# Kernel optimization log

Hardware: AMD Instinct MI355X
Metric: run time of the kernel (lower is better)

## Reference

```python
import jax, jax.numpy as jnp
import numpy as np

B, N, D, H, FF, K, L = 8, 4096, 128, 8, 512, 16, 2
DH = D // H
EPS = 1e-5


def setup_inputs() -> dict:
    key = jax.random.key(0)
    ks = jax.random.split(key, 32)
    s = 0.02
    inp = {
        "x": jax.random.normal(ks[0], (B, N, 8), dtype=jnp.float32),
        "xyz_w": jax.random.normal(ks[1], (D, 3), jnp.float32) * s,
        "xyz_b": jnp.zeros((D,), jnp.float32),
        "ohe_w": jax.random.normal(ks[2], (D, 5), jnp.float32) * s,
        "ohe_b": jnp.zeros((D,), jnp.float32),
        # per-layer transformer params stacked on leading L axis
        "in_proj_w": jax.random.normal(ks[3], (L, 3 * D, D), jnp.float32) * s,
        "in_proj_b": jnp.zeros((L, 3 * D), jnp.float32),
        "out_proj_w": jax.random.normal(ks[4], (L, D, D), jnp.float32) * s,
        "out_proj_b": jnp.zeros((L, D), jnp.float32),
        "ln1_w": jnp.ones((L, D), jnp.float32),
        "ln1_b": jnp.zeros((L, D), jnp.float32),
        "lin1_w": jax.random.normal(ks[5], (L, FF, D), jnp.float32) * s,
        "lin1_b": jnp.zeros((L, FF), jnp.float32),
        "lin2_w": jax.random.normal(ks[6], (L, D, FF), jnp.float32) * s,
        "lin2_b": jnp.zeros((L, D), jnp.float32),
        "ln2_w": jnp.ones((L, D), jnp.float32),
        "ln2_b": jnp.zeros((L, D), jnp.float32),
        "fc1_w": jax.random.normal(ks[7], (FF, D), jnp.float32) * s,
        "fc1_b": jnp.zeros((FF,), jnp.float32),
        "fc2_w": jax.random.normal(ks[8], (1, FF), jnp.float32) * s,
        "fc2_b": jnp.zeros((1,), jnp.float32),
    }
    return inp


def _layer_norm(x, w, b):
    m = jnp.mean(x, -1, keepdims=True)
    v = jnp.mean((x - m) ** 2, -1, keepdims=True)
    return (x - m) * jax.lax.rsqrt(v + EPS) * w + b


def _knn_attention(xyz, feat):
    # squared euclidean distances preserve top-k ordering of cdist(p=2)
    d2 = jnp.sum((xyz[:, :, None, :] - xyz[:, None, :, :]) ** 2, -1)  # [B,N,N]
    _, idx = jax.lax.top_k(-d2, K + 1)  # ascending distance
    idx = idx[..., 1:]  # drop self -> [B,N,K]
    knn = jax.vmap(lambda f, i: f[i])(feat, idx)  # [B,N,K,D]
    scale = 1.0 / np.sqrt(D)
    scores = jnp.einsum('bnd,bnkd->bnk', feat, knn) * scale
    w = jax.nn.softmax(scores, -1)
    return jnp.einsum('bnk,bnkd->bnd', w, knn)


def _mha(x, in_w, in_b, out_w, out_b):
    qkv = x @ in_w.T + in_b  # [B,N,3D]
    q, k, v = jnp.split(qkv, 3, axis=-1)
    def heads(t):
        return t.reshape(B, N, H, DH).transpose(0, 2, 1, 3)  # [B,H,N,DH]
    q, k, v = heads(q), heads(k), heads(v)
    scores = jnp.einsum('bhqd,bhkd->bhqk', q, k) / np.sqrt(DH)
    a = jax.nn.softmax(scores, -1)
    o = jnp.einsum('bhqk,bhkd->bhqd', a, v).transpose(0, 2, 1, 3).reshape(B, N, D)
    return o @ out_w.T + out_b


def reference(x, xyz_w, xyz_b, ohe_w, ohe_b, in_proj_w, in_proj_b, out_proj_w,
              out_proj_b, ln1_w, ln1_b, lin1_w, lin1_b, lin2_w, lin2_b,
              ln2_w, ln2_b, fc1_w, fc1_b, fc2_w, fc2_b):
    xyz = x[:, :, :3]
    ohe = x[:, :, 3:8]
    feat = (xyz @ xyz_w.T + xyz_b) + (ohe @ ohe_w.T + ohe_b)  # [B,N,D]
    h = _knn_attention(xyz, feat)
    # post-norm TransformerEncoder (PyTorch default, relu, no dropout at eval)
    for l in range(L):
        a = _mha(h, in_proj_w[l], in_proj_b[l], out_proj_w[l], out_proj_b[l])
        h = _layer_norm(h + a, ln1_w[l], ln1_b[l])
        f = jax.nn.relu(h @ lin1_w[l].T + lin1_b[l]) @ lin2_w[l].T + lin2_b[l]
        h = _layer_norm(h + f, ln2_w[l], ln2_b[l])
    pooled = jnp.mean(h, axis=1)  # [B,D]
    out = jax.nn.sigmoid(jax.nn.relu(pooled @ fc1_w.T + fc1_b) @ fc2_w.T + fc2_b)
    return out
```

## Files before the change

### kernel.cpp

```cpp
#include <hip/hip_runtime.h>

#define Bq 8
#define Nq 4096
#define Dq 128
#define Hq 8
#define FFq 512
#define KNNq 16
#define Lq 2
#define DHq 16
#define EPSq 1e-5f

typedef _Float16 half4 __attribute__((ext_vector_type(4)));
typedef _Float16 half2t __attribute__((ext_vector_type(2)));
typedef float v4f __attribute__((ext_vector_type(4)));

static __device__ __forceinline__ half2t pkrtz(float a, float b) {
    return __builtin_bit_cast(half2t, __builtin_amdgcn_cvt_pkrtz(a, b));
}

__global__ __launch_bounds__(256) void prep_kernel(const float* __restrict__ x,
                                                   const float* __restrict__ xyz_w,
                                                   const float* __restrict__ xyz_b,
                                                   const float* __restrict__ ohe_w,
                                                   const float* __restrict__ ohe_b,
                                                   _Float16* __restrict__ feat16,
                                                   const float* __restrict__ ipw,
                                                   const float* __restrict__ opw,
                                                   const float* __restrict__ l1w,
                                                   const float* __restrict__ l2w,
                                                   _Float16* __restrict__ wb) {
    int bid = blockIdx.x;
    if (bid < 16384) {
        int i = bid * 256 + threadIdx.x;
        int d = i & 127;
        int t = i >> 7;
        const float* xr = x + (size_t)t * 8;
        float s = xyz_b[d] + ohe_b[d];
        s += xr[0] * xyz_w[d * 3 + 0] + xr[1] * xyz_w[d * 3 + 1] + xr[2] * xyz_w[d * 3 + 2];
        s += xr[3] * ohe_w[d * 5 + 0] + xr[4] * ohe_w[d * 5 + 1] + xr[5] * ohe_w[d * 5 + 2]
           + xr[6] * ohe_w[d * 5 + 3] + xr[7] * ohe_w[d * 5 + 4];
        feat16[i] = (_Float16)s;
    } else {
        int i = (bid - 16384) * 256 + threadIdx.x;
        float v;
        if (i < 98304) v = ipw[i];
        else if (i < 131072) v = opw[i - 98304];
        else if (i < 262144) v = l1w[i - 131072];
        else v = l2w[i - 262144];
        wb[i] = (_Float16)v;
    }
}

__global__ __launch_bounds__(512) void knn_kernel(const float* __restrict__ x, int* __restrict__ idx) {
    __shared__ __attribute__((aligned(16))) float sx[Nq];
    __shared__ __attribute__((aligned(16))) float sy[Nq];
    __shared__ __attribute__((aligned(16))) float sz[Nq];
    unsigned int (*md)[17] = (unsigned int (*)[17])sx;
    int b = blockIdx.y;
    int tid = threadIdx.x;
    for (int p = tid; p < Nq; p += 512) {
        const float* xr = x + ((size_t)b * Nq + p) * 8;
        sx[p] = xr[0]; sy[p] = xr[1]; sz[p] = xr[2];
    }
    __syncthreads();
    int qi = tid >> 3;
    int part = tid & 7;
    int n = blockIdx.x * 64 + qi;
    float qx = sx[n], qy = sy[n], qz = sz[n];
    unsigned int top[16];
#pragma unroll
    for (int i = 0; i < 16; i++) top[i] = 0xFFFFFFFFu;
    int j0 = part * 512;
    int rot = part;
    for (int bb = 0; bb < 32; bb++) {
        unsigned int c[16];
#pragma unroll
        for (int u = 0; u < 16; u++) {
            int j = j0 + ((bb * 16 + rot + u) & 511);
            float px = sx[j], py = sy[j], pz = sz[j];
            float dx = qx - px, dy = qy - py, dz = qz - pz;
            float d2 = fmaf(dx, dx, fmaf(dy, dy, dz * dz));
            unsigned int ky = (__float_as_uint(d2) & 0xFFFFF000u) | (unsigned int)j;
            c[u] = (j == n) ? 0xFFFFFFFFu : ky;
        }
#pragma unroll
        for (int kk = 2; kk <= 16; kk <<= 1) {
#pragma unroll
            for (int jj = 16 >> 1; jj > 0; jj >>= 1) {
                if (jj < kk) {
#pragma unroll
                    for (int i = 0; i < 16; i++) {
                        int l = i ^ jj;
                        if (l > i) {
                            unsigned int a0 = c[i], b0 = c[l];
                            unsigned int mn = a0 < b0 ? a0 : b0;
                            unsigned int mx = a0 < b0 ? b0 : a0;
                            bool up = ((i & kk) == 0);
                            c[i] = up ? mn : mx;
                            c[l] = up ? mx : mn;
                        }
                    }
                }
            }
        }
#pragma unroll
        for (int i = 0; i < 16; i++) {
            unsigned int a0 = top[i], b0 = c[15 - i];
            top[i] = a0 < b0 ? a0 : b0;
        }
#pragma unroll
        for (int d = 8; d >= 1; d >>= 1) {
#pragma unroll
            for (int i = 0; i < 16; i++) {
                if ((i & d) == 0) {
                    int l = i | d;
                    unsigned int a0 = top[i], b0 = top[l];
                    top[i] = a0 < b0 ? a0 : b0;
                    top[l] = a0 < b0 ? b0 : a0;
                }
            }
        }
    }
    __syncthreads();
#pragma unroll
    for (int i = 0; i < 16; i++) md[tid][i] = top[i];
    __syncthreads();
    if (part == 0) {
        unsigned int pall = 0;
        int* op = idx + ((size_t)b * Nq + n) * KNNq;
        int base_row = qi * 8;
#pragma unroll
        for (int s = 0; s < KNNq; s++) {
            unsigned int best = 0xFFFFFFFFu; int bp = 0;
#pragma unroll
            for (int p2 = 0; p2 < 8; p2++) {
                unsigned int ptr = (pall >> (p2 * 4)) & 15u;
                unsigned int v = md[base_row + p2][ptr];
                if (v < best) { best = v; bp = p2; }
            }
            op[s] = (int)(best & 4095u);
            pall += (1u << (bp * 4));
        }
    }
}

__global__ __launch_bounds__(256, 4) void knn_attn_kernel(const _Float16* __restrict__ feat16,
                                                          const int* __restrict__ idx,
                                                          _Float16* __restrict__ h16) {
    int wave = threadIdx.x >> 6;
    int lane = threadIdx.x & 63;
    int token = blockIdx.x * 4 + wave;
    int b = token >> 12;
    half2t fh = ((const half2t*)(feat16 + (size_t)token * Dq))[lane];
    float2 f = make_float2((float)fh[0], (float)fh[1]);
    const int* ip = idx + (size_t)token * KNNq;
    int jj[KNNq];
#pragma unroll
    for (int k = 0; k < KNNq; k++) jj[k] = ip[k];
    float2 g[KNNq];
#pragma unroll
    for (int k = 0; k < KNNq; k++) {
        half2t gh = ((const half2t*)(feat16 + (((size_t)b << 12) + jj[k]) * Dq))[lane];
        g[k] = make_float2((float)gh[0], (float)gh[1]);
    }
    float sc[KNNq];
#pragma unroll
    for (int k = 0; k < KNNq; k++) {
        float p = f.x * g[k].x + f.y * g[k].y;
#pragma unroll
        for (int m = 1; m < 64; m <<= 1) p += __shfl_xor(p, m);
        sc[k] = p * 0.088388347648318447f;
    }
    float mx = sc[0];
#pragma unroll
    for (int k = 1; k < KNNq; k++) mx = fmaxf(mx, sc[k]);
    float sum = 0.f;
#pragma unroll
    for (int k = 0; k < KNNq; k++) { sc[k] = __expf(sc[k] - mx); sum += sc[k]; }
    float inv = 1.f / sum;
    float o0 = 0.f, o1 = 0.f;
#pragma unroll
    for (int k = 0; k < KNNq; k++) { o0 += sc[k] * g[k].x; o1 += sc[k] * g[k].y; }
    ((half2t*)(h16 + (size_t)token * Dq))[lane] = pkrtz(o0 * inv, o1 * inv);
}

template <int MODE>
__global__ __launch_bounds__(256) void hgemm_kernel(const _Float16* __restrict__ A,
                                                    const _Float16* __restrict__ W,
                                                    const float* __restrict__ bias,
                                                    void* __restrict__ Cout,
                                                    int M, int Nc, int K) {
    int tid = threadIdx.x;
    int lane = tid & 63, w = tid >> 6;
    int l15 = lane & 15, l4 = lane >> 4;
    int m0 = blockIdx.y * 64 + w * 16;
    int n0 = blockIdx.x * 64;
    const _Float16* Ap = A + (size_t)(m0 + l15) * K + l4 * 4;
    const _Float16* Wp = W + (size_t)(n0 + l15) * K + l4 * 4;
    v4f acc[4] = {{0.f, 0.f, 0.f, 0.f}, {0.f, 0.f, 0.f, 0.f}, {0.f, 0.f, 0.f, 0.f}, {0.f, 0.f, 0.f, 0.f}};
    for (int ks = 0; ks < K; ks += 16) {
        half4 af = *(const half4*)(Ap + ks);
#pragma unroll
        for (int nt = 0; nt < 4; nt++) {
            half4 wf = *(const half4*)(Wp + (size_t)nt * 16 * K + ks);
            acc[nt] = __builtin_amdgcn_mfma_f32_16x16x16f16(wf, af, acc[nt], 0, 0, 0);
        }
    }
    int m = m0 + l15;
#pragma unroll
    for (int nt = 0; nt < 4; nt++) {
        int nb = n0 + nt * 16 + l4 * 4;
        float4 bv = *(const float4*)(bias + nb);
        float v0 = acc[nt][0] + bv.x, v1 = acc[nt][1] + bv.y;
        float v2 = acc[nt][2] + bv.z, v3 = acc[nt][3] + bv.w;
        int n_base = n0 + nt * 16;
        int sel = n_base >> 7;
        if (MODE == 2 && sel == 0) {
            v0 *= 0.36067376f; v1 *= 0.36067376f; v2 *= 0.36067376f; v3 *= 0.36067376f;
        }
        half2t lo = pkrtz(v0, v1);
        half2t hi = pkrtz(v2, v3);
        half4 hv; hv[0] = lo[0]; hv[1] = lo[1]; hv[2] = hi[0]; hv[3] = hi[1];
        if (sel < 2) {
            int hh = (n_base >> 4) & 7;
            size_t base = (size_t)sel * (64ull * Nq * 16)
                        + ((size_t)((m >> 12) * 8 + hh)) * (Nq * 16)
                        + (size_t)(m & 4095) * 16 + l4 * 4;
            *(half4*)((_Float16*)Cout + base) = hv;
        } else {
            int hh = (n_base >> 4) & 7;
            size_t vb = 2ull * 64 * Nq * 16
                      + ((size_t)((m >> 12) * 8 + hh)) * (16 * Nq)
                      + (size_t)(m & 4095);
            _Float16* vp = (_Float16*)Cout + vb + (size_t)(l4 * 4) * Nq;
            vp[0 * Nq] = hv[0]; vp[1 * Nq] = hv[1]; vp[2 * Nq] = hv[2]; vp[3 * Nq] = hv[3];
        }
    }
}

__global__ __launch_bounds__(256) void flash12_kernel(const _Float16* __restrict__ pk,
                                                      _Float16* __restrict__ out16) {
    __shared__ _Float16 Ks[2][64 * 20];
    __shared__ _Float16 Vs[2][16 * 66];
    int tid = threadIdx.x;
    int lane = tid & 63, w = tid >> 6;
    int bh = blockIdx.y;
    const _Float16* Qb = pk + (size_t)bh * (Nq * 16);
    const _Float16* Kb = pk + (size_t)(64 + bh) * (Nq * 16);
    const _Float16* Vt = pk + 2ull * 64 * Nq * 16 + (size_t)bh * (16 * Nq);
    int q0 = blockIdx.x * 128 + w * 32;
    int l15 = lane & 15, l4 = lane >> 4;

    half4 qfA = *(const half4*)(Qb + (size_t)(q0 + l15) * 16 + l4 * 4);
    half4 qfB = *(const half4*)(Qb + (size_t)(q0 + 16 + l15) * 16 + l4 * 4);

    int sr = tid >> 2, sc = tid & 3;
    int vd = tid >> 4, vj = (tid & 15) * 4;
    const _Float16* Kg = Kb + (size_t)sr * 16 + sc * 4;
    const _Float16* Vg = Vt + (size_t)vd * Nq + vj;

    *(half4*)(Ks[0] + sr * 20 + sc * 4) = *(const half4*)(Kg);
    *(half4*)(Vs[0] + vd * 66 + vj) = *(const half4*)(Vg);
    __syncthreads();

    v4f oA = {0.f, 0.f, 0.f, 0.f}, oB = {0.f, 0.f, 0.f, 0.f};
    v4f lacA = {0.f, 0.f, 0.f, 0.f}, lacB = {0.f, 0.f, 0.f, 0.f};
    half4 ones;
    ones[0] = ones[1] = ones[2] = ones[3] = (_Float16)1.0f;

    for (int kt = 0; kt < Nq / 64; kt++) {
        int cur = kt & 1, nxt = cur ^ 1;
        if (kt < Nq / 64 - 1) {
            *(half4*)(Ks[nxt] + sr * 20 + sc * 4) = *(const half4*)(Kg + (size_t)(kt + 1) * 64 * 16);
            *(half4*)(Vs[nxt] + vd * 66 + vj) = *(const half4*)(Vg + (kt + 1) * 64);
        }
        half4 kf[4];
#pragma unroll
        for (int g = 0; g < 4; g++)
            kf[g] = *(const half4*)(Ks[cur] + (g * 16 + l15) * 20 + l4 * 4);
        v4f SA[4], SB[4];
#pragma unroll
        for (int g = 0; g < 4; g++) {
            SA[g] = __builtin_amdgcn_mfma_f32_16x16x16f16(kf[g], qfA, (v4f){0.f, 0.f, 0.f, 0.f}, 0, 0, 0);
            SB[g] = __builtin_amdgcn_mfma_f32_16x16x16f16(kf[g], qfB, (v4f){0.f, 0.f, 0.f, 0.f}, 0, 0, 0);
        }
        half4 PA[4], PB[4];
#pragma unroll
        for (int g = 0; g < 4; g++) {
            float a0 = __builtin_amdgcn_exp2f(SA[g][0]);
            float a1 = __builtin_amdgcn_exp2f(SA[g][1]);
            float a2 = __builtin_amdgcn_exp2f(SA[g][2]);
            float a3 = __builtin_amdgcn_exp2f(SA[g][3]);
            half2t alo = pkrtz(a0, a1);
            half2t ahi = pkrtz(a2, a3);
            PA[g][0] = alo[0]; PA[g][1] = alo[1]; PA[g][2] = ahi[0]; PA[g][3] = ahi[1];
            float b0 = __builtin_amdgcn_exp2f(SB[g][0]);
            float b1 = __builtin_amdgcn_exp2f(SB[g][1]);
            float b2 = __builtin_amdgcn_exp2f(SB[g][2]);
            float b3 = __builtin_amdgcn_exp2f(SB[g][3]);
            half2t blo = pkrtz(b0, b1);
            half2t bhi = pkrtz(b2, b3);
            PB[g][0] = blo[0]; PB[g][1] = blo[1]; PB[g][2] = bhi[0]; PB[g][3] = bhi[1];
        }
#pragma unroll
        for (int g = 0; g < 4; g++) {
            half4 vf = *(const half4*)(Vs[cur] + l15 * 66 + g * 16 + l4 * 4);
            lacA = __builtin_amdgcn_mfma_f32_16x16x16f16(ones, PA[g], lacA, 0, 0, 0);
            oA = __builtin_amdgcn_mfma_f32_16x16x16f16(vf, PA[g], oA, 0, 0, 0);
            lacB = __builtin_amdgcn_mfma_f32_16x16x16f16(ones, PB[g], lacB, 0, 0, 0);
            oB = __builtin_amdgcn_mfma_f32_16x16x16f16(vf, PB[g], oB, 0, 0, 0);
        }
        __syncthreads();
    }
    int b = bh >> 3, hh = bh & 7;
    {
        float inv = 1.f / lacA[0];
        int row = q0 + l15;
        half2t lo = pkrtz(oA[0] * inv, oA[1] * inv);
        half2t hi = pkrtz(oA[2] * inv, oA[3] * inv);
        half4 hv; hv[0] = lo[0]; hv[1] = lo[1]; hv[2] = hi[0]; hv[3] = hi[1];
        *(half4*)(out16 + ((size_t)(b * Nq + row)) * Dq + hh * 16 + l4 * 4) = hv;
    }
    {
        float inv = 1.f / lacB[0];
        int row = q0 + 16 + l15;
        half2t lo = pkrtz(oB[0] * inv, oB[1] * inv);
        half2t hi = pkrtz(oB[2] * inv, oB[3] * inv);
        half4 hv; hv[0] = lo[0]; hv[1] = lo[1]; hv[2] = hi[0]; hv[3] = hi[1];
        *(half4*)(out16 + ((size_t)(b * Nq + row)) * Dq + hh * 16 + l4 * 4) = hv;
    }
}

__global__ __launch_bounds__(256) void hgemm_ln_kernel(const _Float16* __restrict__ A,
                                                       const _Float16* __restrict__ W,
                                                       const float* __restrict__ bias,
                                                       const float* __restrict__ lnw,
                                                       const float* __restrict__ lnb,
                                                       _Float16* __restrict__ h16,
                                                       int K) {
    int tid = threadIdx.x;
    int lane = tid & 63, w = tid >> 6;
    int l15 = lane & 15, l4 = lane >> 4;
    int m0 = blockIdx.x * 64 + w * 16;
    const _Float16* Ap = A + (size_t)(m0 + l15) * K + l4 * 4;
    const _Float16* Wp = W + (size_t)l15 * K + l4 * 4;
    v4f acc[8] = {};
    for (int ks = 0; ks < K; ks += 16) {
        half4 af = *(const half4*)(Ap + ks);
#pragma unroll
        for (int nt = 0; nt < 8; nt++) {
            half4 wf = *(const half4*)(Wp + (size_t)nt * 16 * K + ks);
            acc[nt] = __builtin_amdgcn_mfma_f32_16x16x16f16(wf, af, acc[nt], 0, 0, 0);
        }
    }
    int m = m0 + l15;
    float x[8][4];
    float psum = 0.f;
#pragma unroll
    for (int nt = 0; nt < 8; nt++) {
        int nb = nt * 16 + l4 * 4;
        float4 bv = *(const float4*)(bias + nb);
        half4 rv = *(const half4*)(h16 + (size_t)m * Dq + nb);
        x[nt][0] = acc[nt][0] + bv.x + (float)rv[0];
        x[nt][1] = acc[nt][1] + bv.y + (float)rv[1];
        x[nt][2] = acc[nt][2] + bv.z + (float)rv[2];
        x[nt][3] = acc[nt][3] + bv.w + (float)rv[3];
        psum += (x[nt][0] + x[nt][1]) + (x[nt][2] + x[nt][3]);
    }
    psum += __shfl_xor(psum, 16);
    psum += __shfl_xor(psum, 32);
    float mean = psum * (1.f / 128.f);
    float vsum = 0.f;
#pragma unroll
    for (int nt = 0; nt < 8; nt++)
#pragma unroll
        for (int r = 0; r < 4; r++) {
            x[nt][r] -= mean;
            vsum += x[nt][r] * x[nt][r];
        }
    vsum += __shfl_xor(vsum, 16);
    vsum += __shfl_xor(vsum, 32);
    float inv = rsqrtf(vsum * (1.f / 128.f) + EPSq);
#pragma unroll
    for (int nt = 0; nt < 8; nt++) {
        int nb = nt * 16 + l4 * 4;
        float4 wv = *(const float4*)(lnw + nb);
        float4 bb = *(const float4*)(lnb + nb);
        float y0 = x[nt][0] * inv * wv.x + bb.x;
        float y1 = x[nt][1] * inv * wv.y + bb.y;
        float y2 = x[nt][2] * inv * wv.z + bb.z;
        float y3 = x[nt][3] * inv * wv.w + bb.w;
        half2t lo = pkrtz(y0, y1);
        half2t hi = pkrtz(y2, y3);
        half4 hv2; hv2[0] = lo[0]; hv2[1] = lo[1]; hv2[2] = hi[0]; hv2[3] = hi[1];
        *(half4*)(h16 + (size_t)m * Dq + nb) = hv2;
    }
}

template <int LAST>
__global__ __launch_bounds__(256) void ffn_kernel(const _Float16* __restrict__ h16in,
                                                  const _Float16* __restrict__ W1,
                                                  const float* __restrict__ b1,
                                                  const _Float16* __restrict__ W2,
                                                  const float* __restrict__ b2,
                                                  const float* __restrict__ lnw,
                                                  const float* __restrict__ lnb,
                                                  _Float16* __restrict__ h16,
                                                  float* __restrict__ part) {
    int tid = threadIdx.x;
    int lane = tid & 63, w = tid >> 6;
    int l15 = lane & 15, l4 = lane >> 4;
    int m0 = blockIdx.x * 64 + w * 16;
    int m = m0 + l15;
    const _Float16* Ap = h16in + (size_t)m * Dq + l4 * 4;
    half4 afr[8];
#pragma unroll
    for (int t = 0; t < 8; t++) afr[t] = *(const half4*)(Ap + t * 16);
    half4 mid[32];
#pragma unroll
    for (int c = 0; c < 8; c++) {
        v4f acc[4] = {};
#pragma unroll
        for (int t = 0; t < 8; t++) {
#pragma unroll
            for (int nt = 0; nt < 4; nt++) {
                half4 wf = *(const half4*)(W1 + (size_t)(c * 64 + nt * 16 + l15) * 128 + t * 16 + l4 * 4);
                acc[nt] = __builtin_amdgcn_mfma_f32_16x16x16f16(wf, afr[t], acc[nt], 0, 0, 0);
            }
        }
#pragma unroll
        for (int nt = 0; nt < 4; nt++) {
            float4 bv = *(const float4*)(b1 + c * 64 + nt * 16 + l4 * 4);
            float v0 = fmaxf(acc[nt][0] + bv.x, 0.f);
            float v1 = fmaxf(acc[nt][1] + bv.y, 0.f);
            float v2 = fmaxf(acc[nt][2] + bv.z, 0.f);
            float v3 = fmaxf(acc[nt][3] + bv.w, 0.f);
            half2t lo = pkrtz(v0, v1), hi = pkrtz(v2, v3);
            half4 hv; hv[0] = lo[0]; hv[1] = lo[1]; hv[2] = hi[0]; hv[3] = hi[1];
            mid[c * 4 + nt] = hv;
        }
    }
    v4f acc8[8] = {};
#pragma unroll 4
    for (int t = 0; t < 32; t++) {
#pragma unroll
        for (int nt = 0; nt < 8; nt++) {
            half4 wf = *(const half4*)(W2 + (size_t)(nt * 16 + l15) * 512 + t * 16 + l4 * 4);
            acc8[nt] = __builtin_amdgcn_mfma_f32_16x16x16f16(wf, mid[t], acc8[nt], 0, 0, 0);
        }
    }
    float x[8][4];
    float psum = 0.f;
#pragma unroll
    for (int nt = 0; nt < 8; nt++) {
        int nb = nt * 16 + l4 * 4;
        float4 bv = *(const float4*)(b2 + nb);
        x[nt][0] = acc8[nt][0] + bv.x + (float)afr[nt][0];
        x[nt][1] = acc8[nt][1] + bv.y + (float)afr[nt][1];
        x[nt][2] = acc8[nt][2] + bv.z + (float)afr[nt][2];
        x[nt][3] = acc8[nt][3] + bv.w + (float)afr[nt][3];
        psum += (x[nt][0] + x[nt][1]) + (x[nt][2] + x[nt][3]);
    }
    psum += __shfl_xor(psum, 16);
    psum += __shfl_xor(psum, 32);
    float mean = psum * (1.f / 128.f);
    float vsum = 0.f;
#pragma unroll
    for (int nt = 0; nt < 8; nt++)
#pragma unroll
        for (int r = 0; r < 4; r++) {
            x[nt][r] -= mean;
            vsum += x[nt][r] * x[nt][r];
        }
    vsum += __shfl_xor(vsum, 16);
    vsum += __shfl_xor(vsum, 32);
    float inv = rsqrtf(vsum * (1.f / 128.f) + EPSq);
#pragma unroll
    for (int nt = 0; nt < 8; nt++) {
        int nb = nt * 16 + l4 * 4;
        float4 wv = *(const float4*)(lnw + nb);
        float4 bb = *(const float4*)(lnb + nb);
        x[nt][0] = x[nt][0] * inv * wv.x + bb.x;
        x[nt][1] = x[nt][1] * inv * wv.y + bb.y;
        x[nt][2] = x[nt][2] * inv * wv.z + bb.z;
        x[nt][3] = x[nt][3] * inv * wv.w + bb.w;
        if (!LAST) {
            half2t lo = pkrtz(x[nt][0], x[nt][1]);
            half2t hi = pkrtz(x[nt][2], x[nt][3]);
            half4 hv2; hv2[0] = lo[0]; hv2[1] = lo[1]; hv2[2] = hi[0]; hv2[3] = hi[1];
            *(half4*)(h16 + (size_t)m * Dq + nb) = hv2;
        }
    }
    if (LAST) {
#pragma unroll
        for (int nt = 0; nt < 8; nt++)
#pragma unroll
            for (int r = 0; r < 4; r++) {
                float v = x[nt][r];
                v += __shfl_xor(v, 1);
                v += __shfl_xor(v, 2);
                v += __shfl_xor(v, 4);
                v += __shfl_xor(v, 8);
                x[nt][r] = v;
            }
        if (l15 == 0) {
            float* pp = part + ((size_t)blockIdx.x * 4 + w) * Dq;
#pragma unroll
            for (int nt = 0; nt < 8; nt++)
#pragma unroll
                for (int r = 0; r < 4; r++)
                    pp[nt * 16 + l4 * 4 + r] = x[nt][r];
        }
    }
}

__global__ __launch_bounds__(512) void head_kernel(const float* __restrict__ part,
                                                   const float* __restrict__ fc1_w, const float* __restrict__ fc1_b,
                                                   const float* __restrict__ fc2_w, const float* __restrict__ fc2_b,
                                                   float* __restrict__ out) {
    __shared__ float psh[Dq];
    __shared__ float red[512];
    int b = blockIdx.x, f = threadIdx.x;
    if (f < Dq) {
        float s = 0.f;
        for (int c = 0; c < 256; c++) s += part[((size_t)b * 256 + c) * Dq + f];
        psh[f] = s * (1.f / 4096.f);
    }
    __syncthreads();
    const float* wr = fc1_w + (size_t)f * Dq;
    float s = fc1_b[f];
    for (int d = 0; d < Dq; d++) s += psh[d] * wr[d];
    red[f] = fmaxf(s, 0.f) * fc2_w[f];
    __syncthreads();
    for (int st = 256; st > 0; st >>= 1) {
        if (f < st) red[f] += red[f + st];
        __syncthreads();
    }
    if (f == 0) out[b] = 1.f / (1.f + __expf(-(red[0] + fc2_b[0])));
}

extern "C" void kernel_launch(void* const* d_in, const int* in_sizes, int n_in,
                              void* d_out, int out_size, void* d_ws, size_t ws_size,
                              hipStream_t stream) {
    const float* x        = (const float*)d_in[0];
    const float* xyz_w    = (const float*)d_in[1];
    const float* xyz_b    = (const float*)d_in[2];
    const float* ohe_w    = (const float*)d_in[3];
    const float* ohe_b    = (const float*)d_in[4];
    const float* in_proj_w  = (const float*)d_in[5];
    const float* in_proj_b  = (const float*)d_in[6];
    const float* out_proj_w = (const float*)d_in[7];
    const float* out_proj_b = (const float*)d_in[8];
    const float* ln1_w    = (const float*)d_in[9];
    const float* ln1_b    = (const float*)d_in[10];
    const float* lin1_w   = (const float*)d_in[11];
    const float* lin1_b   = (const float*)d_in[12];
    const float* lin2_w   = (const float*)d_in[13];
    const float* lin2_b   = (const float*)d_in[14];
    const float* ln2_w    = (const float*)d_in[15];
    const float* ln2_b    = (const float*)d_in[16];
    const float* fc1_w    = (const float*)d_in[17];
    const float* fc1_b    = (const float*)d_in[18];
    const float* fc2_w    = (const float*)d_in[19];
    const float* fc2_b    = (const float*)d_in[20];
    float* outp = (float*)d_out;

    char* ws = (char*)d_ws;
    size_t off = 0;
    auto alloc = [&](size_t bytes) { void* p = ws + off; off += (bytes + 255) & ~255ULL; return p; };
    _Float16*  feat16 = (_Float16*)alloc((size_t)Bq * Nq * Dq * 2);
    _Float16*  h16    = (_Float16*)alloc((size_t)Bq * Nq * Dq * 2);
    _Float16*  abuf16 = (_Float16*)alloc((size_t)Bq * Nq * Dq * 2);
    _Float16*  pkb    = (_Float16*)alloc(3ull * 64 * Nq * 16 * 2);
    _Float16*  wb     = (_Float16*)alloc(393216ull * 2);
    int*       idx    = (int*)alloc((size_t)Bq * Nq * KNNq * 4);
    float*     part   = (float*)alloc(2048ull * Dq * 4);
    if (off > ws_size) return;

    const _Float16* wip16 = wb;
    const _Float16* wop16 = wb + 98304;
    const _Float16* wl116 = wb + 131072;
    const _Float16* wl216 = wb + 262144;

    int M = Bq * Nq;

    prep_kernel<<<16384 + 1536, 256, 0, stream>>>(x, xyz_w, xyz_b, ohe_w, ohe_b, feat16,
                                                  in_proj_w, out_proj_w, lin1_w, lin2_w, wb);
    knn_kernel<<<dim3(Nq / 64, Bq), 512, 0, stream>>>(x, idx);
    knn_attn_kernel<<<M / 4, 256, 0, stream>>>(feat16, idx, h16);

    for (int l = 0; l < Lq; l++) {
        hgemm_kernel<2><<<dim3(384 / 64, M / 64), 256, 0, stream>>>(
            h16, wip16 + (size_t)l * 384 * 128, in_proj_b + l * 384, pkb, M, 384, 128);
        flash12_kernel<<<dim3(Nq / 128, Bq * Hq), 256, 0, stream>>>(pkb, abuf16);
        hgemm_ln_kernel<<<M / 64, 256, 0, stream>>>(
            abuf16, wop16 + (size_t)l * 128 * 128, out_proj_b + l * 128,
            ln1_w + l * 128, ln1_b + l * 128, h16, 128);
        if (l == 0) {
            ffn_kernel<0><<<M / 64, 256, 0, stream>>>(
                h16, wl116, lin1_b, wl216, lin2_b, ln2_w, ln2_b, h16, part);
        } else {
            ffn_kernel<1><<<M / 64, 256, 0, stream>>>(
                h16, wl116 + (size_t)l * 512 * 128, lin1_b + l * 512,
                wl216 + (size_t)l * 128 * 512, lin2_b + l * 128,
                ln2_w + l * 128, ln2_b + l * 128, h16, part);
        }
    }

    head_kernel<<<Bq, 512, 0, stream>>>(part, fc1_w, fc1_b, fc2_w, fc2_b, outp);
}
```

Baseline: 1.018 ms.

## Fuse out-projection+LayerNorm into FFN kernel and drop self-exclusion in kNN

Merges the out-proj GEMM with LN1 and the FFN with LN2 into a single kernel, so the LN1 output stays in registers as the MFMA A-fragment. This removes one launch and one round trip of h16 through global memory per layer. Separately, the kNN inner loop no longer compares every candidate against the query index. Instead it takes the 17 nearest and drops the first, which assumes the self point always sorts first at distance zero. Register pressure in the fused kernel rises, which could lower occupancy.

New measurement: 1.010 ms. Within noise of the previous version (-0.8%).

```diff
diff --git a/kernel.cpp b/kernel.cpp
--- a/kernel.cpp
+++ b/kernel.cpp
@@ -80,8 +80,7 @@
             float px = sx[j], py = sy[j], pz = sz[j];
             float dx = qx - px, dy = qy - py, dz = qz - pz;
             float d2 = fmaf(dx, dx, fmaf(dy, dy, dz * dz));
-            unsigned int ky = (__float_as_uint(d2) & 0xFFFFF000u) | (unsigned int)j;
-            c[u] = (j == n) ? 0xFFFFFFFFu : ky;
+            c[u] = (__float_as_uint(d2) & 0xFFFFF000u) | (unsigned int)j;
         }
 #pragma unroll
         for (int kk = 2; kk <= 16; kk <<= 1) {
@@ -124,22 +123,23 @@
     __syncthreads();
 #pragma unroll
     for (int i = 0; i < 16; i++) md[tid][i] = top[i];
+    md[tid][16] = 0xFFFFFFFFu;
     __syncthreads();
     if (part == 0) {
-        unsigned int pall = 0;
+        unsigned long long pall = 0;
         int* op = idx + ((size_t)b * Nq + n) * KNNq;
         int base_row = qi * 8;
 #pragma unroll
-        for (int s = 0; s < KNNq; s++) {
+        for (int s = 0; s < KNNq + 1; s++) {
             unsigned int best = 0xFFFFFFFFu; int bp = 0;
 #pragma unroll
             for (int p2 = 0; p2 < 8; p2++) {
-                unsigned int ptr = (pall >> (p2 * 4)) & 15u;
+                unsigned int ptr = (unsigned int)((pall >> (p2 * 5)) & 31u);
                 unsigned int v = md[base_row + p2][ptr];
                 if (v < best) { best = v; bp = p2; }
             }
-            op[s] = (int)(best & 4095u);
-            pall += (1u << (bp * 4));
+            if (s > 0) op[s - 1] = (int)(best & 4095u);
+            pall += (1ull << (bp * 5));
         }
     }
 }
@@ -331,35 +331,43 @@
     }
 }
 
-__global__ __launch_bounds__(256) void hgemm_ln_kernel(const _Float16* __restrict__ A,
-                                                       const _Float16* __restrict__ W,
-                                                       const float* __restrict__ bias,
-                                                       const float* __restrict__ lnw,
-                                                       const float* __restrict__ lnb,
-                                                       _Float16* __restrict__ h16,
-                                                       int K) {
+template <int LAST>
+__global__ __launch_bounds__(256) void oln_ffn_kernel(const _Float16* __restrict__ A,
+                                                      const _Float16* __restrict__ Wo,
+                                                      const float* __restrict__ bo,
+                                                      const float* __restrict__ ln1w,
+                                                      const float* __restrict__ ln1b,
+                                                      const _Float16* __restrict__ W1,
+                                                      const float* __restrict__ b1,
+                                                      const _Float16* __restrict__ W2,
+                                                      const float* __restrict__ b2,
+                                                      const float* __restrict__ ln2w,
+                                                      const float* __restrict__ ln2b,
+                                                      _Float16* __restrict__ h16,
+                                                      float* __restrict__ part) {
     int tid = threadIdx.x;
     int lane = tid & 63, w = tid >> 6;
     int l15 = lane & 15, l4 = lane >> 4;
     int m0 = blockIdx.x * 64 + w * 16;
-    const _Float16* Ap = A + (size_t)(m0 + l15) * K + l4 * 4;
-    const _Float16* Wp = W + (size_t)l15 * K + l4 * 4;
+    int m = m0 + l15;
+
+    const _Float16* Ap = A + (size_t)m * 128 + l4 * 4;
+    const _Float16* Wp = Wo + (size_t)l15 * 128 + l4 * 4;
     v4f acc[8] = {};
-    for (int ks = 0; ks < K; ks += 16) {
+    for (int ks = 0; ks < 128; ks += 16) {
         half4 af = *(const half4*)(Ap + ks);
 #pragma unroll
         for (int nt = 0; nt < 8; nt++) {
-            half4 wf = *(const half4*)(Wp + (size_t)nt * 16 * K + ks);
+            half4 wf = *(const half4*)(Wp + (size_t)nt * 16 * 128 + ks);
             acc[nt] = __builtin_amdgcn_mfma_f32_16x16x16f16(wf, af, acc[nt], 0, 0, 0);
         }
     }
-    int m = m0 + l15;
     float x[8][4];
     float psum = 0.f;
 #pragma unroll
     for (int nt = 0; nt < 8; nt++) {
         int nb = nt * 16 + l4 * 4;
-        float4 bv = *(const float4*)(bias + nb);
+        float4 bv = *(const float4*)(bo + nb);
         half4 rv = *(const half4*)(h16 + (size_t)m * Dq + nb);
         x[nt][0] = acc[nt][0] + bv.x + (float)rv[0];
         x[nt][1] = acc[nt][1] + bv.y + (float)rv[1];
@@ -380,61 +388,41 @@
         }
     vsum += __shfl_xor(vsum, 16);
     vsum += __shfl_xor(vsum, 32);
-    float inv = rsqrtf(vsum * (1.f / 128.f) + EPSq);
+    float inv1 = rsqrtf(vsum * (1.f / 128.f) + EPSq);
+    half4 afr[8];
 #pragma unroll
     for (int nt = 0; nt < 8; nt++) {
         int nb = nt * 16 + l4 * 4;
-        float4 wv = *(const float4*)(lnw + nb);
-        float4 bb = *(const float4*)(lnb + nb);
-        float y0 = x[nt][0] * inv * wv.x + bb.x;
-        float y1 = x[nt][1] * inv * wv.y + bb.y;
-        float y2 = x[nt][2] * inv * wv.z + bb.z;
-        float y3 = x[nt][3] * inv * wv.w + bb.w;
+        float4 wv = *(const float4*)(ln1w + nb);
+        float4 bb = *(const float4*)(ln1b + nb);
+        float y0 = x[nt][0] * inv1 * wv.x + bb.x;
+        float y1 = x[nt][1] * inv1 * wv.y + bb.y;
+        float y2 = x[nt][2] * inv1 * wv.z + bb.z;
+        float y3 = x[nt][3] * inv1 * wv.w + bb.w;
         half2t lo = pkrtz(y0, y1);
         half2t hi = pkrtz(y2, y3);
-        half4 hv2; hv2[0] = lo[0]; hv2[1] = lo[1]; hv2[2] = hi[0]; hv2[3] = hi[1];
-        *(half4*)(h16 + (size_t)m * Dq + nb) = hv2;
-    }
-}
-
-template <int LAST>
-__global__ __launch_bounds__(256) void ffn_kernel(const _Float16* __restrict__ h16in,
-                                                  const _Float16* __restrict__ W1,
-                                                  const float* __restrict__ b1,
-                                                  const _Float16* __restrict__ W2,
-                                                  const float* __restrict__ b2,
-                                                  const float* __restrict__ lnw,
-                                                  const float* __restrict__ lnb,
-                                                  _Float16* __restrict__ h16,
-                                                  float* __restrict__ part) {
-    int tid = threadIdx.x;
-    int lane = tid & 63, w = tid >> 6;
-    int l15 = lane & 15, l4 = lane >> 4;
-    int m0 = blockIdx.x * 64 + w * 16;
-    int m = m0 + l15;
-    const _Float16* Ap = h16in + (size_t)m * Dq + l4 * 4;
-    half4 afr[8];
-#pragma unroll
-    for (int t = 0; t < 8; t++) afr[t] = *(const half4*)(Ap + t * 16);
+        afr[nt][0] = lo[0]; afr[nt][1] = lo[1]; afr[nt][2] = hi[0]; afr[nt][3] = hi[1];
+    }
+
     half4 mid[32];
 #pragma unroll
     for (int c = 0; c < 8; c++) {
-        v4f acc[4] = {};
+        v4f accm[4] = {};
 #pragma unroll
         for (int t = 0; t < 8; t++) {
 #pragma unroll
             for (int nt = 0; nt < 4; nt++) {
                 half4 wf = *(const half4*)(W1 + (size_t)(c * 64 + nt * 16 + l15) * 128 + t * 16 + l4 * 4);
-                acc[nt] = __builtin_amdgcn_mfma_f32_16x16x16f16(wf, afr[t], acc[nt], 0, 0, 0);
+                accm[nt] = __builtin_amdgcn_mfma_f32_16x16x16f16(wf, afr[t], accm[nt], 0, 0, 0);
             }
         }
 #pragma unroll
         for (int nt = 0; nt < 4; nt++) {
             float4 bv = *(const float4*)(b1 + c * 64 + nt * 16 + l4 * 4);
-            float v0 = fmaxf(acc[nt][0] + bv.x, 0.f);
-            float v1 = fmaxf(acc[nt][1] + bv.y, 0.f);
-            float v2 = fmaxf(acc[nt][2] + bv.z, 0.f);
-            float v3 = fmaxf(acc[nt][3] + bv.w, 0.f);
+            float v0 = fmaxf(accm[nt][0] + bv.x, 0.f);
+            float v1 = fmaxf(accm[nt][1] + bv.y, 0.f);
+            float v2 = fmaxf(accm[nt][2] + bv.z, 0.f);
+            float v3 = fmaxf(accm[nt][3] + bv.w, 0.f);
             half2t lo = pkrtz(v0, v1), hi = pkrtz(v2, v3);
             half4 hv; hv[0] = lo[0]; hv[1] = lo[1]; hv[2] = hi[0]; hv[3] = hi[1];
             mid[c * 4 + nt] = hv;
@@ -449,44 +437,44 @@
             acc8[nt] = __builtin_amdgcn_mfma_f32_16x16x16f16(wf, mid[t], acc8[nt], 0, 0, 0);
         }
     }
-    float x[8][4];
-    float psum = 0.f;
+    float x2[8][4];
+    float psum2 = 0.f;
 #pragma unroll
     for (int nt = 0; nt < 8; nt++) {
         int nb = nt * 16 + l4 * 4;
         float4 bv = *(const float4*)(b2 + nb);
-        x[nt][0] = acc8[nt][0] + bv.x + (float)afr[nt][0];
-        x[nt][1] = acc8[nt][1] + bv.y + (float)afr[nt][1];
-        x[nt][2] = acc8[nt][2] + bv.z + (float)afr[nt][2];
-        x[nt][3] = acc8[nt][3] + bv.w + (float)afr[nt][3];
-        psum += (x[nt][0] + x[nt][1]) + (x[nt][2] + x[nt][3]);
-    }
-    psum += __shfl_xor(psum, 16);
-    psum += __shfl_xor(psum, 32);
-    float mean = psum * (1.f / 128.f);
-    float vsum = 0.f;
+        x2[nt][0] = acc8[nt][0] + bv.x + (float)afr[nt][0];
+        x2[nt][1] = acc8[nt][1] + bv.y + (float)afr[nt][1];
+        x2[nt][2] = acc8[nt][2] + bv.z + (float)afr[nt][2];
+        x2[nt][3] = acc8[nt][3] + bv.w + (float)afr[nt][3];
+        psum2 += (x2[nt][0] + x2[nt][1]) + (x2[nt][2] + x2[nt][3]);
+    }
+    psum2 += __shfl_xor(psum2, 16);
+    psum2 += __shfl_xor(psum2, 32);
+    float mean2 = psum2 * (1.f / 128.f);
+    float vsum2 = 0.f;
 #pragma unroll
     for (int nt = 0; nt < 8; nt++)
 #pragma unroll
         for (int r = 0; r < 4; r++) {
-            x[nt][r] -= mean;
-            vsum += x[nt][r] * x[nt][r];
-        }
-    vsum += __shfl_xor(vsum, 16);
-    vsum += __shfl_xor(vsum, 32);
-    float inv = rsqrtf(vsum * (1.f / 128.f) + EPSq);
+            x2[nt][r] -= mean2;
+            vsum2 += x2[nt][r] * x2[nt][r];
+        }
+    vsum2 += __shfl_xor(vsum2, 16);
+    vsum2 += __shfl_xor(vsum2, 32);
+    float inv2 = rsqrtf(vsum2 * (1.f / 128.f) + EPSq);
 #pragma unroll
     for (int nt = 0; nt < 8; nt++) {
         int nb = nt * 16 + l4 * 4;
-        float4 wv = *(const float4*)(lnw + nb);
-        float4 bb = *(const float4*)(lnb + nb);
-        x[nt][0] = x[nt][0] * inv * wv.x + bb.x;
-        x[nt][1] = x[nt][1] * inv * wv.y + bb.y;
-        x[nt][2] = x[nt][2] * inv * wv.z + bb.z;
-        x[nt][3] = x[nt][3] * inv * wv.w + bb.w;
+        float4 wv = *(const float4*)(ln2w + nb);
+        float4 bb = *(const float4*)(ln2b + nb);
+        x2[nt][0] = x2[nt][0] * inv2 * wv.x + bb.x;
+        x2[nt][1] = x2[nt][1] * inv2 * wv.y + bb.y;
+        x2[nt][2] = x2[nt][2] * inv2 * wv.z + bb.z;
+        x2[nt][3] = x2[nt][3] * inv2 * wv.w + bb.w;
         if (!LAST) {
-            half2t lo = pkrtz(x[nt][0], x[nt][1]);
-            half2t hi = pkrtz(x[nt][2], x[nt][3]);
+            half2t lo = pkrtz(x2[nt][0], x2[nt][1]);
+            half2t hi = pkrtz(x2[nt][2], x2[nt][3]);
             half4 hv2; hv2[0] = lo[0]; hv2[1] = lo[1]; hv2[2] = hi[0]; hv2[3] = hi[1];
             *(half4*)(h16 + (size_t)m * Dq + nb) = hv2;
         }
@@ -496,12 +484,12 @@
         for (int nt = 0; nt < 8; nt++)
 #pragma unroll
             for (int r = 0; r < 4; r++) {
-                float v = x[nt][r];
+                float v = x2[nt][r];
                 v += __shfl_xor(v, 1);
                 v += __shfl_xor(v, 2);
                 v += __shfl_xor(v, 4);
                 v += __shfl_xor(v, 8);
-                x[nt][r] = v;
+                x2[nt][r] = v;
             }
         if (l15 == 0) {
             float* pp = part + ((size_t)blockIdx.x * 4 + w) * Dq;
@@ -509,7 +497,7 @@
             for (int nt = 0; nt < 8; nt++)
 #pragma unroll
                 for (int r = 0; r < 4; r++)
-                    pp[nt * 16 + l4 * 4 + r] = x[nt][r];
+                    pp[nt * 16 + l4 * 4 + r] = x2[nt][r];
         }
     }
 }
@@ -593,15 +581,17 @@
         hgemm_kernel<2><<<dim3(384 / 64, M / 64), 256, 0, stream>>>(
             h16, wip16 + (size_t)l * 384 * 128, in_proj_b + l * 384, pkb, M, 384, 128);
         flash12_kernel<<<dim3(Nq / 128, Bq * Hq), 256, 0, stream>>>(pkb, abuf16);
-        hgemm_ln_kernel<<<M / 64, 256, 0, stream>>>(
-            abuf16, wop16 + (size_t)l * 128 * 128, out_proj_b + l * 128,
-            ln1_w + l * 128, ln1_b + l * 128, h16, 128);
         if (l == 0) {
-            ffn_kernel<0><<<M / 64, 256, 0, stream>>>(
-                h16, wl116, lin1_b, wl216, lin2_b, ln2_w, ln2_b, h16, part);
+            oln_ffn_kernel<0><<<M / 64, 256, 0, stream>>>(
+                abuf16, wop16, out_proj_b,
+                ln1_w, ln1_b,
+                wl116, lin1_b, wl216, lin2_b,
+                ln2_w, ln2_b, h16, part);
         } else {
-            ffn_kernel<1><<<M / 64, 256, 0, stream>>>(
-                h16, wl116 + (size_t)l * 512 * 128, lin1_b + l * 512,
+            oln_ffn_kernel<1><<<M / 64, 256, 0, stream>>>(
+                abuf16, wop16 + (size_t)l * 128 * 128, out_proj_b + l * 128,
+                ln1_w + l * 128, ln1_b + l * 128,
+                wl116 + (size_t)l * 512 * 128, lin1_b + l * 512,
                 wl216 + (size_t)l * 128 * 512, lin2_b + l * 128,
                 ln2_w + l * 128, ln2_b + l * 128, h16, part);
         }
```
